# Kernel optimization log

Measured on AMD Instinct MI355X. Metric: run time of the kernel, lower is better.

The kernel has to match this reference:

```python
import jax, jax.numpy as jnp
import numpy as np

N = 50000
E = 800000
C_IN = 64
C_OUT = 64
K = 3  # Chebyshev order (num_stacks)
LAMBDA_MAX = 2.0


def setup_inputs() -> dict:
    key = jax.random.key(0)
    ks = jax.random.split(key, 32)
    inp = {
        'X': jax.random.normal(ks[0], (N, C_IN), dtype=jnp.float32),
        'edge_index': jax.random.randint(ks[1], (2, E), 0, N, dtype=jnp.int64),
        'edge_weight': jax.random.uniform(ks[2], (E,), dtype=jnp.float32),
        'H': jax.random.normal(ks[3], (N, C_OUT), dtype=jnp.float32),
        'C': jax.random.normal(ks[4], (N, C_OUT), dtype=jnp.float32),
    }
    # 8 ChebConvs: conv_{x,h}_{i,f,c,o}; x-convs map C_IN->C_OUT, h-convs C_OUT->C_OUT
    names_x = ['Wxi', 'Wxf', 'Wxc', 'Wxo']
    names_h = ['Whi', 'Whf', 'Whc', 'Who']
    i = 5
    for nx, nh in zip(names_x, names_h):
        inp[nx] = jax.random.normal(ks[i], (K, C_IN, C_OUT), dtype=jnp.float32) * (1.0 / np.sqrt(K * C_IN)); i += 1
        inp['b' + nx[1:]] = jax.random.normal(ks[i], (C_OUT,), dtype=jnp.float32) * 0.01; i += 1
        inp[nh] = jax.random.normal(ks[i], (K, C_OUT, C_OUT), dtype=jnp.float32) * (1.0 / np.sqrt(K * C_OUT)); i += 1
        inp['b' + nh[1:]] = jax.random.normal(ks[i], (C_OUT,), dtype=jnp.float32) * 0.01; i += 1
    # per-gate biases b_i, b_f, b_c, b_o of shape [1, C_OUT] (zero-initialized in torch)
    for nm in ['bi', 'bf', 'bc', 'bo']:
        inp[nm] = jax.random.normal(ks[i], (1, C_OUT), dtype=jnp.float32) * 0.01; i += 1
    return inp


def _cheb_norm(edge_index, edge_weight, n):
    # symmetric normalization: D^-1/2 W D^-1/2 (PyG get_laplacian 'sym')
    row, col = edge_index[0], edge_index[1]
    deg = jax.ops.segment_sum(edge_weight, row, num_segments=n)
    dinv = jnp.where(deg > 0, jax.lax.rsqrt(jnp.where(deg > 0, deg, 1.0)), 0.0)
    return dinv[row] * edge_weight * dinv[col]


def _cheb_conv(x, W, b, row, col, nw, n):
    # ChebConv: out = sum_k T_k(L_hat) x @ W[k] + b, with
    # L_hat v = (2/lambda_max) * (v - A_norm v) - v
    def Lhat(v):
        agg = jax.ops.segment_sum(nw[:, None] * v[col], row, num_segments=n)
        return (2.0 / LAMBDA_MAX) * (v - agg) - v
    Tx_prev = x
    out = x @ W[0]
    k = W.shape[0]
    if k > 1:
        Tx = Lhat(x)
        out = out + Tx @ W[1]
        for j in range(2, k):
            Tx_new = 2.0 * Lhat(Tx) - Tx_prev
            out = out + Tx_new @ W[j]
            Tx_prev, Tx = Tx, Tx_new
    return out + b


def reference(X, edge_index, edge_weight, H, C,
              Wxi, bxi, Whi, bhi, Wxf, bxf, Whf, bhf,
              Wxc, bxc, Whc, bhc, Wxo, bxo, Who, bho,
              bi, bf, bc, bo):
    n = X.shape[0]
    row, col = edge_index[0], edge_index[1]
    nw = _cheb_norm(edge_index, edge_weight, n)
    cc = lambda v, W, b: _cheb_conv(v, W, b, row, col, nw, n)
    I = jax.nn.sigmoid(cc(X, Wxi, bxi) + cc(H, Whi, bhi) + bi)
    F = jax.nn.sigmoid(cc(X, Wxf, bxf) + cc(H, Whf, bhf) + bf)
    T = jnp.tanh(cc(X, Wxc, bxc) + cc(H, Whc, bhc) + bc)
    C_new = F * C + I * T
    O = jax.nn.sigmoid(cc(X, Wxo, bxo) + cc(H, Who, bho) + bo)
    H_new = O * jnp.tanh(C_new)
    return (H_new, C_new)
```

## Files before the change

### kernel.cpp

```cpp
#include <hip/hip_runtime.h>

#define N_NODES 50000
#define N_PAD   50048
#define N_EDGES 800000
#define NBE     3125
#define NB_IL   6250

typedef __attribute__((ext_vector_type(8))) short bf16x8;
typedef __attribute__((ext_vector_type(4))) float f32x4;

__device__ __forceinline__ unsigned short f2bf(float f) {
    unsigned u = __float_as_uint(f);
    u = (u + 0x7fffu + ((u >> 16) & 1u)) >> 16;
    return (unsigned short)u;
}

__device__ __forceinline__ float fsig(float x) {
    x = fminf(fmaxf(x, -30.f), 30.f);
    float t = __expf(x);
    return __fdividef(t, 1.f + t);
}
__device__ __forceinline__ float ftanh(float x) {
    x = fminf(fmaxf(x, -15.f), 15.f);
    float t = __expf(2.f * x);
    return 1.f - __fdividef(2.f, t + 1.f);
}

__device__ __forceinline__ int block_is_i32(const int* __restrict__ eiv, int t, int* sflag) {
    if (t == 0) *sflag = 0;
    __syncthreads();
    int v = eiv[1 + 2 * t];
    if (v) atomicOr(sflag, 1);
    __syncthreads();
    return *sflag;
}


__global__ __launch_bounds__(256) void k_deg_prep(
    const void* __restrict__ eiraw, const float* __restrict__ w,
    unsigned long long* __restrict__ packed, unsigned* __restrict__ rank,
    const float* __restrict__ X, const float* __restrict__ H, unsigned short* __restrict__ XH,
    const float* __restrict__ Wxi, const float* __restrict__ Whi,
    const float* __restrict__ Wxf, const float* __restrict__ Whf,
    const float* __restrict__ Wxc, const float* __restrict__ Whc,
    const float* __restrict__ Wxo, const float* __restrict__ Who,
    const float* __restrict__ bxi, const float* __restrict__ bhi,
    const float* __restrict__ bxf, const float* __restrict__ bhf,
    const float* __restrict__ bxc, const float* __restrict__ bhc,
    const float* __restrict__ bxo, const float* __restrict__ bho,
    const float* __restrict__ bgi, const float* __restrict__ bgf,
    const float* __restrict__ bgc, const float* __restrict__ bgo,
    unsigned short* __restrict__ Wf, float* __restrict__ ball) {
    __shared__ int sflag;
    int b = blockIdx.x, t = threadIdx.x;
    if (b < NBE) {
        int is32 = block_is_i32((const int*)eiraw, t, &sflag);
        int e = b * 256 + t;
        if (e >= N_EDGES) return;
        int r = is32 ? ((const int*)eiraw)[e] : (int)(((const long long*)eiraw)[e]);
        unsigned qw = (unsigned)(w[e] * 4194304.f + 0.5f);
        unsigned long long old = atomicAdd(&packed[r], (1ull << 32) | (unsigned long long)qw);
        rank[e] = (unsigned)(old >> 32);
        return;
    }
    int bb = b - NBE;
    if (bb < NB_IL) {
        int tt = bb * 256 + t;
        int node = tt >> 5, g = tt & 31;
        float4 v = (g < 16) ? *(const float4*)(X + (size_t)node * 64 + g * 4)
                            : *(const float4*)(H + (size_t)node * 64 + (g - 16) * 4);
        ushort4 o;
        o.x = f2bf(v.x); o.y = f2bf(v.y); o.z = f2bf(v.z); o.w = f2bf(v.w);
        *(ushort4*)(XH + (size_t)node * 128 + g * 4) = o;
        return;
    }
    bb -= NB_IL;
    if (bb < 48) {
        int flat = bb * 256 + t;
        int l = flat & 63, nt = (flat >> 6) & 15, ks = flat >> 10;
        int n = nt * 16 + (l & 15);
        int g = n >> 6, c = n & 63;
        const float* WX = (g == 0) ? Wxi : (g == 1) ? Wxf : (g == 2) ? Wxc : Wxo;
        const float* WH = (g == 0) ? Whi : (g == 1) ? Whf : (g == 2) ? Whc : Who;
        int k0 = ks * 32 + (l >> 4) * 8;
        unsigned short ov[8];
#pragma unroll
        for (int j = 0; j < 8; j++) {
            int k = k0 + j;
            int bsel = k >> 7, ch = k & 127;
            const float* W = (ch < 64) ? WX : WH;
            int kk = ch & 63;
            float v;
            if (bsel == 0)      v = W[kk * 64 + c] - W[2 * 4096 + kk * 64 + c];
            else if (bsel == 1) v = -W[4096 + kk * 64 + c];
            else                v = 2.f * W[2 * 4096 + kk * 64 + c];
            ov[j] = f2bf(v);
        }
        uint4 o;
        o.x = (unsigned)ov[0] | ((unsigned)ov[1] << 16);
        o.y = (unsigned)ov[2] | ((unsigned)ov[3] << 16);
        o.z = (unsigned)ov[4] | ((unsigned)ov[5] << 16);
        o.w = (unsigned)ov[6] | ((unsigned)ov[7] << 16);
        *(uint4*)(Wf + (size_t)flat * 8) = o;
    } else {
        int g = t >> 6, c = t & 63;
        const float* BX = (g == 0) ? bxi : (g == 1) ? bxf : (g == 2) ? bxc : bxo;
        const float* BH = (g == 0) ? bhi : (g == 1) ? bhf : (g == 2) ? bhc : bho;
        const float* BG = (g == 0) ? bgi : (g == 1) ? bgf : (g == 2) ? bgc : bgo;
        ball[t] = BX[c] + BH[c] + BG[c];
    }
}


__global__ __launch_bounds__(256) void k_scan1(const unsigned long long* __restrict__ packed,
                                               int* __restrict__ rp, int* __restrict__ part,
                                               float* __restrict__ dinv) {
    __shared__ int s[256];
    int t = threadIdx.x, i = blockIdx.x * 256 + t;
    unsigned long long p = (i < N_NODES) ? packed[i] : 0ull;
    int v = (int)(p >> 32);
    s[t] = v; __syncthreads();
    for (int d = 1; d < 256; d <<= 1) {
        int add = (t >= d) ? s[t - d] : 0;
        __syncthreads();
        s[t] += add;
        __syncthreads();
    }
    if (i < N_NODES) {
        rp[i] = s[t] - v;
        float dg = (float)(unsigned)(p & 0xffffffffu) * (1.f / 4194304.f);
        dinv[i] = (dg > 0.f) ? rsqrtf(dg) : 0.f;
        if (i == N_NODES - 1) rp[N_NODES] = s[t];
    }
    if (t == 255) part[blockIdx.x] = s[255];
}

__global__ __launch_bounds__(256) void k_scan2(int* __restrict__ part, int nb) {
    __shared__ int s[256];
    int t = threadIdx.x;
    int v = (t < nb) ? part[t] : 0;
    s[t] = v; __syncthreads();
    for (int d = 1; d < 256; d <<= 1) {
        int add = (t >= d) ? s[t - d] : 0;
        __syncthreads();
        s[t] += add;
        __syncthreads();
    }
    if (t < nb) part[t] = s[t] - v;
}

__global__ __launch_bounds__(256) void k_scatter(const void* __restrict__ eiraw, const float* __restrict__ w,
                                                 const unsigned* __restrict__ rank,
                                                 const float* __restrict__ dinv, const int* __restrict__ rp,
                                                 const int* __restrict__ part,
                                                 int* __restrict__ colp, float* __restrict__ nwp) {
    __shared__ int sflag;
    int t = threadIdx.x;
    int is32 = block_is_i32((const int*)eiraw, t, &sflag);
    int e = blockIdx.x * 256 + t;
    if (e >= N_EDGES) return;
    int r, c;
    if (is32) { r = ((const int*)eiraw)[e]; c = ((const int*)eiraw)[N_EDGES + e]; }
    else      { r = (int)(((const long long*)eiraw)[e]); c = (int)(((const long long*)eiraw)[N_EDGES + e]); }
    int pos = rp[r] + part[r >> 8] + (int)rank[e];
    colp[pos] = c;
    nwp[pos] = dinv[r] * w[e] * dinv[c];
}


__global__ __launch_bounds__(256) void k_spmv_bf(const unsigned short* __restrict__ src,
                                                 unsigned short* __restrict__ dst,
                                                 const int* __restrict__ rp, const int* __restrict__ part,
                                                 const int* __restrict__ colp, const float* __restrict__ nwp) {
    int wid = threadIdx.x >> 6, lane = threadIdx.x & 63;
    int node = blockIdx.x * 4 + wid;
    if (node >= N_NODES) return;
    int s = rp[node] + part[node >> 8];
    int e = rp[node + 1] + part[(node + 1) >> 8];
    float a0 = 0.f, a1 = 0.f;
    for (int jb = s; jb < e; jb += 8) {
        int   c[8]; float wv[8]; unsigned vv[8];
#pragma unroll
        for (int k = 0; k < 8; k++) {
            int j = jb + k;
            int jc = (j < e) ? j : (e - 1);
            c[k]  = colp[jc];
            wv[k] = (j < e) ? nwp[jc] : 0.f;
        }
#pragma unroll
        for (int k = 0; k < 8; k++)
            vv[k] = *(const unsigned*)(src + (size_t)c[k] * 128 + lane * 2);
#pragma unroll
        for (int k = 0; k < 8; k++) {
            a0 = fmaf(wv[k], __uint_as_float(vv[k] << 16), a0);
            a1 = fmaf(wv[k], __uint_as_float(vv[k] & 0xffff0000u), a1);
        }
    }
    unsigned o = (unsigned)f2bf(a0) | ((unsigned)f2bf(a1) << 16);
    *(unsigned*)(dst + (size_t)node * 128 + lane * 2) = o;
}


__global__ __launch_bounds__(256) void k_gemm_mfma(
    const unsigned short* __restrict__ XH, const unsigned short* __restrict__ U1,
    const unsigned short* __restrict__ U2, const unsigned short* __restrict__ Wf,
    const float* __restrict__ ball, const float* __restrict__ C, float* __restrict__ out) {
    __shared__ __align__(16) uint4 Bs[2][1024];

    int t = threadIdx.x;
    int wid = t >> 6, lane = t & 63;
    int col = lane & 15, quad = lane >> 4;
    int m0 = blockIdx.x * 64 + wid * 16;
    int arow = m0 + col;

    f32x4 acc[16];
#pragma unroll
    for (int i = 0; i < 16; i++) acc[i] = (f32x4){0.f, 0.f, 0.f, 0.f};

    const unsigned short* srcs[3] = {XH, U1, U2};

    bf16x8 a_cur = *(const bf16x8*)(srcs[0] + (size_t)arow * 128 + quad * 8);
    const uint4* g0 = (const uint4*)Wf;
    uint4 p0 = g0[t], p1 = g0[t + 256], p2 = g0[t + 512], p3 = g0[t + 768];

    for (int ks = 0; ks < 12; ks++) {
        uint4* dstb = Bs[ks & 1];
        dstb[t] = p0; dstb[t + 256] = p1; dstb[t + 512] = p2; dstb[t + 768] = p3;
        __syncthreads();
        bf16x8 a_nxt = a_cur;
        if (ks < 11) {
            int ks1 = ks + 1;
            const uint4* g = (const uint4*)(Wf + (size_t)ks1 * 8192);
            p0 = g[t]; p1 = g[t + 256]; p2 = g[t + 512]; p3 = g[t + 768];
            a_nxt = *(const bf16x8*)(srcs[ks1 >> 2] + (size_t)arow * 128 + (ks1 & 3) * 32 + quad * 8);
        }
        const unsigned short* B = (const unsigned short*)Bs[ks & 1];
#pragma unroll
        for (int nt = 0; nt < 16; nt++) {
            bf16x8 bfrag = *(const bf16x8*)(B + nt * 512 + lane * 8);
            acc[nt] = __builtin_amdgcn_mfma_f32_16x16x32_bf16(a_cur, bfrag, acc[nt], 0, 0, 0);
        }
        a_cur = a_nxt;
    }

    float bI[4], bF[4], bT[4], bO[4];
#pragma unroll
    for (int cq = 0; cq < 4; cq++) {
        int c = cq * 16 + col;
        bI[cq] = ball[c]; bF[cq] = ball[64 + c]; bT[cq] = ball[128 + c]; bO[cq] = ball[192 + c];
    }
#pragma unroll
    for (int r = 0; r < 4; r++) {
        int node = m0 + quad * 4 + r;
        if (node >= N_NODES) continue;
#pragma unroll
        for (int cq = 0; cq < 4; cq++) {
            int c = cq * 16 + col;
            float ig = fsig(acc[0 + cq][r]  + bI[cq]);
            float fg = fsig(acc[4 + cq][r]  + bF[cq]);
            float tg = ftanh(acc[8 + cq][r] + bT[cq]);
            float og = fsig(acc[12 + cq][r] + bO[cq]);
            float cv = fmaf(fg, C[(size_t)node * 64 + c], ig * tg);
            out[(size_t)node * 64 + c] = og * ftanh(cv);
            out[(size_t)N_NODES * 64 + (size_t)node * 64 + c] = cv;
        }
    }
}


extern "C" void kernel_launch(void* const* d_in, const int* in_sizes, int n_in,
                              void* d_out, int out_size, void* d_ws, size_t ws_size,
                              hipStream_t stream) {
    const float* X   = (const float*)d_in[0];
    const void*  ei  = d_in[1];
    const float* w   = (const float*)d_in[2];
    const float* H   = (const float*)d_in[3];
    const float* C   = (const float*)d_in[4];
    const float* Wxi = (const float*)d_in[5];  const float* bxi = (const float*)d_in[6];
    const float* Whi = (const float*)d_in[7];  const float* bhi = (const float*)d_in[8];
    const float* Wxf = (const float*)d_in[9];  const float* bxf = (const float*)d_in[10];
    const float* Whf = (const float*)d_in[11]; const float* bhf = (const float*)d_in[12];
    const float* Wxc = (const float*)d_in[13]; const float* bxc = (const float*)d_in[14];
    const float* Whc = (const float*)d_in[15]; const float* bhc = (const float*)d_in[16];
    const float* Wxo = (const float*)d_in[17]; const float* bxo = (const float*)d_in[18];
    const float* Who = (const float*)d_in[19]; const float* bho = (const float*)d_in[20];
    const float* bgi = (const float*)d_in[21]; const float* bgf = (const float*)d_in[22];
    const float* bgc = (const float*)d_in[23]; const float* bgo = (const float*)d_in[24];
    float* out = (float*)d_out;

    char* ws = (char*)d_ws;
    size_t off = 0;
    auto alloc = [&](size_t bytes) -> char* {
        char* p = ws + off;
        off = (off + bytes + 255) & ~(size_t)255;
        return p;
    };
    unsigned long long* packed = (unsigned long long*)alloc((size_t)N_NODES * 8);
    unsigned* rank = (unsigned*)alloc((size_t)N_EDGES * 4);
    int*   rp   = (int*)alloc((N_NODES + 1) * 4);
    int*   part = (int*)alloc(256 * 4);
    float* dinv = (float*)alloc(N_NODES * 4);
    int*   colp = (int*)alloc((size_t)(N_EDGES + 8) * 4);
    float* nwp  = (float*)alloc((size_t)(N_EDGES + 8) * 4);
    unsigned short* XH = (unsigned short*)alloc((size_t)N_PAD * 128 * 2);
    unsigned short* U1 = (unsigned short*)alloc((size_t)N_PAD * 128 * 2);
    unsigned short* U2 = (unsigned short*)alloc((size_t)N_PAD * 128 * 2);
    unsigned short* Wf = (unsigned short*)alloc((size_t)12 * 16 * 64 * 8 * 2);
    float* ball = (float*)alloc(256 * 4);
    (void)ws_size; (void)in_sizes; (void)n_in; (void)out_size;

    hipMemsetAsync(packed, 0, (size_t)N_NODES * 8, stream);

    int nbN = (N_NODES + 255) / 256;

    k_deg_prep<<<NBE + NB_IL + 49, 256, 0, stream>>>(ei, w, packed, rank, X, H, XH,
                                                     Wxi, Whi, Wxf, Whf, Wxc, Whc, Wxo, Who,
                                                     bxi, bhi, bxf, bhf, bxc, bhc, bxo, bho,
                                                     bgi, bgf, bgc, bgo, Wf, ball);
    k_scan1<<<nbN, 256, 0, stream>>>(packed, rp, part, dinv);
    k_scan2<<<1, 256, 0, stream>>>(part, nbN);
    k_scatter<<<NBE, 256, 0, stream>>>(ei, w, rank, dinv, rp, part, colp, nwp);
    k_spmv_bf<<<(N_NODES + 3) / 4, 256, 0, stream>>>(XH, U1, rp, part, colp, nwp);
    k_spmv_bf<<<(N_NODES + 3) / 4, 256, 0, stream>>>(U1, U2, rp, part, colp, nwp);
    k_gemm_mfma<<<(N_NODES + 63) / 64, 256, 0, stream>>>(XH, U1, U2, Wf, ball, C, out);
}
```

Baseline: 293.7 us.

## Pack degree atomics into 32-bit words and process four edges per thread

Result: slower. 302.0 us (+2.8%).

```diff
diff --git a/kernel.cpp b/kernel.cpp
--- a/kernel.cpp
+++ b/kernel.cpp
@@ -3,8 +3,8 @@
 #define N_NODES 50000
 #define N_PAD   50048
 #define N_EDGES 800000
-#define NBE     3125
-#define NB_IL   6250
+#define NBE4    782
+#define NB_IL2  1563
 
 typedef __attribute__((ext_vector_type(8))) short bf16x8;
 typedef __attribute__((ext_vector_type(4))) float f32x4;
@@ -26,19 +26,10 @@
     return 1.f - __fdividef(2.f, t + 1.f);
 }
 
-__device__ __forceinline__ int block_is_i32(const int* __restrict__ eiv, int t, int* sflag) {
-    if (t == 0) *sflag = 0;
-    __syncthreads();
-    int v = eiv[1 + 2 * t];
-    if (v) atomicOr(sflag, 1);
-    __syncthreads();
-    return *sflag;
-}
-
 
 __global__ __launch_bounds__(256) void k_deg_prep(
     const void* __restrict__ eiraw, const float* __restrict__ w,
-    unsigned long long* __restrict__ packed, unsigned* __restrict__ rank,
+    unsigned* __restrict__ packed, unsigned* __restrict__ rank,
     const float* __restrict__ X, const float* __restrict__ H, unsigned short* __restrict__ XH,
     const float* __restrict__ Wxi, const float* __restrict__ Whi,
     const float* __restrict__ Wxf, const float* __restrict__ Whf,
@@ -53,28 +44,62 @@
     unsigned short* __restrict__ Wf, float* __restrict__ ball) {
     __shared__ int sflag;
     int b = blockIdx.x, t = threadIdx.x;
-    if (b < NBE) {
-        int is32 = block_is_i32((const int*)eiraw, t, &sflag);
-        int e = b * 256 + t;
-        if (e >= N_EDGES) return;
-        int r = is32 ? ((const int*)eiraw)[e] : (int)(((const long long*)eiraw)[e]);
-        unsigned qw = (unsigned)(w[e] * 4194304.f + 0.5f);
-        unsigned long long old = atomicAdd(&packed[r], (1ull << 32) | (unsigned long long)qw);
-        rank[e] = (unsigned)(old >> 32);
+    if (b < NBE4) {
+        if (t == 0) sflag = 0;
+        __syncthreads();
+        int si = b * 1024 + t;
+        int sv = ((const int*)eiraw)[1 + 2 * si];
+        if (sv) atomicOr(&sflag, 1);
+        __syncthreads();
+        int is32 = sflag;
+
+        int rr[4]; unsigned qq[4]; int ee[4];
+#pragma unroll
+        for (int k = 0; k < 4; k++) {
+            int e = b * 1024 + k * 256 + t;
+            ee[k] = e;
+            if (e < N_EDGES) {
+                rr[k] = is32 ? ((const int*)eiraw)[e] : (int)(((const long long*)eiraw)[e]);
+                qq[k] = (unsigned)(w[e] * 65536.f + 0.5f);
+            } else {
+                rr[k] = -1;
+            }
+        }
+#pragma unroll
+        for (int k = 0; k < 4; k++) {
+            if (rr[k] >= 0) {
+                unsigned old = atomicAdd(&packed[rr[k]], (1u << 22) | qq[k]);
+                rank[ee[k]] = old >> 22;
+            }
+        }
         return;
     }
-    int bb = b - NBE;
-    if (bb < NB_IL) {
+    int bb = b - NBE4;
+    if (bb < NB_IL2) {
         int tt = bb * 256 + t;
-        int node = tt >> 5, g = tt & 31;
-        float4 v = (g < 16) ? *(const float4*)(X + (size_t)node * 64 + g * 4)
-                            : *(const float4*)(H + (size_t)node * 64 + (g - 16) * 4);
-        ushort4 o;
-        o.x = f2bf(v.x); o.y = f2bf(v.y); o.z = f2bf(v.z); o.w = f2bf(v.w);
-        *(ushort4*)(XH + (size_t)node * 128 + g * 4) = o;
+        int node = tt >> 3, g = tt & 7;
+        if (node >= N_NODES) return;
+        const float* base = (g < 4) ? (X + (size_t)node * 64 + g * 16)
+                                    : (H + (size_t)node * 64 + (g - 4) * 16);
+        float4 v0 = ((const float4*)base)[0];
+        float4 v1 = ((const float4*)base)[1];
+        float4 v2 = ((const float4*)base)[2];
+        float4 v3 = ((const float4*)base)[3];
+        uint4 o0, o1;
+        o0.x = (unsigned)f2bf(v0.x) | ((unsigned)f2bf(v0.y) << 16);
+        o0.y = (unsigned)f2bf(v0.z) | ((unsigned)f2bf(v0.w) << 16);
+        o0.z = (unsigned)f2bf(v1.x) | ((unsigned)f2bf(v1.y) << 16);
+        o0.w = (unsigned)f2bf(v1.z) | ((unsigned)f2bf(v1.w) << 16);
+        o1.x = (unsigned)f2bf(v2.x) | ((unsigned)f2bf(v2.y) << 16);
+        o1.y = (unsigned)f2bf(v2.z) | ((unsigned)f2bf(v2.w) << 16);
+        o1.z = (unsigned)f2bf(v3.x) | ((unsigned)f2bf(v3.y) << 16);
+        o1.w = (unsigned)f2bf(v3.z) | ((unsigned)f2bf(v3.w) << 16);
+        unsigned short* dst = XH + (size_t)node * 128 + g * 16;
+        *(uint4*)dst = o0;
+        *(uint4*)(dst + 8) = o1;
         return;
     }
-    bb -= NB_IL;
+    bb -= NB_IL2;
     if (bb < 48) {
         int flat = bb * 256 + t;
         int l = flat & 63, nt = (flat >> 6) & 15, ks = flat >> 10;
@@ -112,13 +137,13 @@
 }
 
 
-__global__ __launch_bounds__(256) void k_scan1(const unsigned long long* __restrict__ packed,
+__global__ __launch_bounds__(256) void k_scan1(const unsigned* __restrict__ packed,
                                                int* __restrict__ rp, int* __restrict__ part,
                                                float* __restrict__ dinv) {
     __shared__ int s[256];
     int t = threadIdx.x, i = blockIdx.x * 256 + t;
-    unsigned long long p = (i < N_NODES) ? packed[i] : 0ull;
-    int v = (int)(p >> 32);
+    unsigned p = (i < N_NODES) ? packed[i] : 0u;
+    int v = (int)(p >> 22);
     s[t] = v; __syncthreads();
     for (int d = 1; d < 256; d <<= 1) {
         int add = (t >= d) ? s[t - d] : 0;
@@ -128,7 +153,7 @@
     }
     if (i < N_NODES) {
         rp[i] = s[t] - v;
-        float dg = (float)(unsigned)(p & 0xffffffffu) * (1.f / 4194304.f);
+        float dg = (float)(p & 0x3fffffu) * (1.f / 65536.f);
         dinv[i] = (dg > 0.f) ? rsqrtf(dg) : 0.f;
         if (i == N_NODES - 1) rp[N_NODES] = s[t];
     }
@@ -155,16 +180,25 @@
                                                  const int* __restrict__ part,
                                                  int* __restrict__ colp, float* __restrict__ nwp) {
     __shared__ int sflag;
-    int t = threadIdx.x;
-    int is32 = block_is_i32((const int*)eiraw, t, &sflag);
-    int e = blockIdx.x * 256 + t;
-    if (e >= N_EDGES) return;
-    int r, c;
-    if (is32) { r = ((const int*)eiraw)[e]; c = ((const int*)eiraw)[N_EDGES + e]; }
-    else      { r = (int)(((const long long*)eiraw)[e]); c = (int)(((const long long*)eiraw)[N_EDGES + e]); }
-    int pos = rp[r] + part[r >> 8] + (int)rank[e];
-    colp[pos] = c;
-    nwp[pos] = dinv[r] * w[e] * dinv[c];
+    int b = blockIdx.x, t = threadIdx.x;
+    if (t == 0) sflag = 0;
+    __syncthreads();
+    int si = b * 1024 + t;
+    int sv = ((const int*)eiraw)[1 + 2 * si];
+    if (sv) atomicOr(&sflag, 1);
+    __syncthreads();
+    int is32 = sflag;
+#pragma unroll
+    for (int k = 0; k < 4; k++) {
+        int e = b * 1024 + k * 256 + t;
+        if (e >= N_EDGES) break;
+        int r, c;
+        if (is32) { r = ((const int*)eiraw)[e]; c = ((const int*)eiraw)[N_EDGES + e]; }
+        else      { r = (int)(((const long long*)eiraw)[e]); c = (int)(((const long long*)eiraw)[N_EDGES + e]); }
+        int pos = rp[r] + part[r >> 8] + (int)rank[e];
+        colp[pos] = c;
+        nwp[pos] = dinv[r] * w[e] * dinv[c];
+    }
 }
 
 
@@ -295,7 +329,7 @@
         off = (off + bytes + 255) & ~(size_t)255;
         return p;
     };
-    unsigned long long* packed = (unsigned long long*)alloc((size_t)N_NODES * 8);
+    unsigned* packed = (unsigned*)alloc((size_t)N_NODES * 4);
     unsigned* rank = (unsigned*)alloc((size_t)N_EDGES * 4);
     int*   rp   = (int*)alloc((N_NODES + 1) * 4);
     int*   part = (int*)alloc(256 * 4);
@@ -309,17 +343,17 @@
     float* ball = (float*)alloc(256 * 4);
     (void)ws_size; (void)in_sizes; (void)n_in; (void)out_size;
 
-    hipMemsetAsync(packed, 0, (size_t)N_NODES * 8, stream);
+    hipMemsetAsync(packed, 0, (size_t)N_NODES * 4, stream);
 
     int nbN = (N_NODES + 255) / 256;
 
-    k_deg_prep<<<NBE + NB_IL + 49, 256, 0, stream>>>(ei, w, packed, rank, X, H, XH,
-                                                     Wxi, Whi, Wxf, Whf, Wxc, Whc, Wxo, Who,
-                                                     bxi, bhi, bxf, bhf, bxc, bhc, bxo, bho,
-                                                     bgi, bgf, bgc, bgo, Wf, ball);
+    k_deg_prep<<<NBE4 + NB_IL2 + 49, 256, 0, stream>>>(ei, w, packed, rank, X, H, XH,
+                                                       Wxi, Whi, Wxf, Whf, Wxc, Whc, Wxo, Who,
+                                                       bxi, bhi, bxf, bhf, bxc, bhc, bxo, bho,
+                                                       bgi, bgf, bgc, bgo, Wf, ball);
     k_scan1<<<nbN, 256, 0, stream>>>(packed, rp, part, dinv);
     k_scan2<<<1, 256, 0, stream>>>(part, nbN);
-    k_scatter<<<NBE, 256, 0, stream>>>(ei, w, rank, dinv, rp, part, colp, nwp);
+    k_scatter<<<NBE4, 256, 0, stream>>>(ei, w, rank, dinv, rp, part, colp, nwp);
     k_spmv_bf<<<(N_NODES + 3) / 4, 256, 0, stream>>>(XH, U1, rp, part, colp, nwp);
     k_spmv_bf<<<(N_NODES + 3) / 4, 256, 0, stream>>>(U1, U2, rp, part, colp, nwp);
     k_gemm_mfma<<<(N_NODES + 63) / 64, 256, 0, stream>>>(XH, U1, U2, Wf, ball, C, out);
```
